# Performance work log

Hardware: AMD Instinct MI355X
Metric: run time of the kernel (lower is better)

Reference implementation:

```python
import jax, jax.numpy as jnp
import numpy as np

ALPHA, BETA, DELTA, TAU, GAMMA = 5.0, 0.6, 0.6, 0.5, 0.5
WINDOW, MOMENTUM = 5, 0.999


def setup_inputs() -> dict:
    key = jax.random.key(0)
    k1, k2 = jax.random.split(key)
    B, C, H, W = 32, 256, 64, 64
    F = jax.random.normal(k1, (B, C, H, W), dtype=jnp.float32)
    S = jnp.eye(C, dtype=jnp.float32)          # EMA similarity buffer (initialized as identity)
    U = jax.random.uniform(k2, (B, C), dtype=jnp.float32)  # replaces torch.bernoulli draw
    return {"F": F, "S": S, "U": U}


def _avg_pool(x, win):
    p = win // 2
    s = jax.lax.reduce_window(x, 0.0, jax.lax.add,
                              (1, 1, win, win), (1, 1, 1, 1),
                              [(0, 0), (0, 0), (p, p), (p, p)])
    return s / (win * win)


def _lrd_mask(F, U):
    # Local Response Density sampling -> boolean mask M [B, C]
    B, C, H, W = F.shape
    a = jax.nn.sigmoid(F.mean(axis=(2, 3)))                     # [B, C]
    max_vals = F.reshape(B, C, -1).max(axis=-1)[:, :, None, None]
    M_bin = (F >= DELTA * max_vals).astype(F.dtype)             # [B, C, H, W]
    density = _avg_pool(M_bin, WINDOW)
    d = (density >= TAU).astype(F.dtype).mean(axis=(2, 3))      # [B, C]
    s = a ** GAMMA * d ** (1.0 - GAMMA)
    s_max = s.max(axis=1, keepdims=True)
    prob = jax.nn.sigmoid(ALPHA * (s - BETA * s_max))
    return U < prob                                             # deterministic bernoulli


def _build_perm(m, S):
    # m: [C] bool selected mask, S: [C, C] similarity -> permutation [C] int32
    C = S.shape[0]
    idx = jnp.arange(C)
    unsel = ~m
    # for each channel, most-similar unselected channel (first max, like torch.argmax)
    masked = jnp.where(unsel[None, :], S, -jnp.inf)
    j = jnp.argmax(masked, axis=1)                              # [C]
    perm = jnp.where(m, j, idx)                                 # perm[selected] = j
    targets = jnp.where(m, j, C)                                # C is out-of-range -> dropped
    perm = perm.at[targets].set(idx, mode='drop')               # perm[j] = selected
    valid = m.any() & unsel.any()
    return jnp.where(valid, perm, idx)


def reference(F, S, U):
    B, C, H, W = F.shape
    # EMA update of channel similarity buffer (no_grad in original)
    F_flat = F.reshape(B, C, -1)
    F_norm = F_flat / (jnp.linalg.norm(F_flat, axis=2, keepdims=True) + 1e-6)
    S_batch = jnp.einsum('bcn,bdn->bcd', F_norm, F_norm).mean(axis=0)
    S_new = jax.lax.stop_gradient(MOMENTUM * S + (1.0 - MOMENTUM) * S_batch)
    # LRD sampling mask and per-sample channel-swap permutation
    M = _lrd_mask(jax.lax.stop_gradient(F), U)                  # [B, C] bool
    perm = jax.vmap(_build_perm, in_axes=(0, None))(M, S_new)   # [B, C]
    # structure-aware channel exchange (gather along channel dim)
    gidx = jnp.broadcast_to(perm[:, :, None, None], (B, C, H, W))
    return jnp.take_along_axis(F, gidx, axis=1)
```

## Files before the change

kernel.cpp:

```cpp
#include <hip/hip_runtime.h>
#include <math.h>

#define BB 32
#define CC 256
#define HH 64
#define WW 64
#define NN 4096

__inline__ __device__ float waveReduceSum(float v) {
    #pragma unroll
    for (int off = 32; off > 0; off >>= 1) v += __shfl_xor(v, off);
    return v;
}
__inline__ __device__ float waveReduceMax(float v) {
    #pragma unroll
    for (int off = 32; off > 0; off >>= 1) v = fmaxf(v, __shfl_xor(v, off));
    return v;
}

__global__ __launch_bounds__(256) void k_prep(const float* __restrict__ F,
                                              float* __restrict__ inv_norm,
                                              float* __restrict__ s_score) {
    const int plane = blockIdx.x;
    const int tid = threadIdx.x;
    __shared__ float bin[4096];
    __shared__ float rowsum[4096];
    __shared__ float swS[4], swQ[4], swM[4];

    const float4* src = (const float4*)(F + (size_t)plane * NN);
    float4 v[4];
    float sum = 0.f, ssq = 0.f, mx = -INFINITY;
    #pragma unroll
    for (int q = 0; q < 4; ++q) {
        v[q] = src[tid + q * 256];
        sum += v[q].x + v[q].y + v[q].z + v[q].w;
        ssq += v[q].x * v[q].x + v[q].y * v[q].y + v[q].z * v[q].z + v[q].w * v[q].w;
        mx = fmaxf(mx, fmaxf(fmaxf(v[q].x, v[q].y), fmaxf(v[q].z, v[q].w)));
    }
    sum = waveReduceSum(sum);
    ssq = waveReduceSum(ssq);
    mx  = waveReduceMax(mx);
    const int w = tid >> 6, ln = tid & 63;
    if (ln == 0) { swS[w] = sum; swQ[w] = ssq; swM[w] = mx; }
    __syncthreads();
    if (tid == 0) {
        swS[0] = swS[0] + swS[1] + swS[2] + swS[3];
        swQ[0] = swQ[0] + swQ[1] + swQ[2] + swQ[3];
        swM[0] = fmaxf(fmaxf(swM[0], swM[1]), fmaxf(swM[2], swM[3]));
    }
    __syncthreads();
    const float totsum = swS[0];
    const float totssq = swQ[0];
    const float thr = 0.6f * swM[0];

    #pragma unroll
    for (int q = 0; q < 4; ++q) {
        const int base = (tid + q * 256) * 4;
        bin[base + 0] = (v[q].x >= thr) ? 1.f : 0.f;
        bin[base + 1] = (v[q].y >= thr) ? 1.f : 0.f;
        bin[base + 2] = (v[q].z >= thr) ? 1.f : 0.f;
        bin[base + 3] = (v[q].w >= thr) ? 1.f : 0.f;
    }
    __syncthreads();

    #pragma unroll
    for (int q = 0; q < 16; ++q) {
        const int p = tid + q * 256;
        const int h = p >> 6, x = p & 63;
        float s5 = 0.f;
        #pragma unroll
        for (int dw = -2; dw <= 2; ++dw) {
            const int xx = x + dw;
            if (xx >= 0 && xx < 64) s5 += bin[h * 64 + xx];
        }
        rowsum[p] = s5;
    }
    __syncthreads();

    int cge = 0;
    #pragma unroll
    for (int q = 0; q < 16; ++q) {
        const int p = tid + q * 256;
        const int h = p >> 6, x = p & 63;
        float cnt = 0.f;
        #pragma unroll
        for (int dh = -2; dh <= 2; ++dh) {
            const int hh = h + dh;
            if (hh >= 0 && hh < 64) cnt += rowsum[hh * 64 + x];
        }
        if (cnt >= 12.5f) cge++;
    }
    float cf = waveReduceSum((float)cge);
    __syncthreads();
    if (ln == 0) swS[w] = cf;
    __syncthreads();
    if (tid == 0) {
        const float total = swS[0] + swS[1] + swS[2] + swS[3];
        const float d = total / 4096.f;
        const float a = 1.f / (1.f + expf(-(totsum / 4096.f)));
        s_score[plane] = sqrtf(a) * sqrtf(d);
        inv_norm[plane] = 1.f / (sqrtf(totssq) + 1e-6f);
    }
}

__global__ __launch_bounds__(256) void k_gram(const float* __restrict__ F,
                                              const float* __restrict__ inv_norm,
                                              float* __restrict__ S_part,
                                              int csh) {
    static const int TI[10] = {0,0,0,0,1,1,1,2,2,3};
    static const int TJ[10] = {0,1,2,3,1,2,3,2,3,3};
    const int t  = blockIdx.x;
    const int bc = blockIdx.y;
    const int b = bc >> csh, chunk = bc & ((1 << csh) - 1);
    const int ti = TI[t], tj = TJ[t];
    const int k0 = chunk << (12 - csh);
    const int iters = 128 >> csh;

    __shared__ float As[32][68];
    __shared__ float Bs[32][68];

    const int tid = threadIdx.x;
    const int lrow = tid >> 2;
    const int kgrp = tid & 3;
    const float* Fb = F + (size_t)b * CC * NN;
    const float scaleA = inv_norm[b * CC + ti * 64 + lrow];
    const float scaleB = inv_norm[b * CC + tj * 64 + lrow];
    const float* gA = Fb + (size_t)(ti * 64 + lrow) * NN + k0 + kgrp * 8;
    const float* gB = Fb + (size_t)(tj * 64 + lrow) * NN + k0 + kgrp * 8;

    const int r0 = (tid >> 4) << 2;
    const int c0 = (tid & 15) << 2;

    float accL2[16];
    #pragma unroll
    for (int e = 0; e < 16; ++e) accL2[e] = 0.f;

    for (int s = 0; s < iters; ++s) {
        const float4 a0 = *(const float4*)(gA);
        const float4 a1 = *(const float4*)(gA + 4);
        const float4 b0 = *(const float4*)(gB);
        const float4 b1 = *(const float4*)(gB + 4);
        __syncthreads();
        const int kb = kgrp * 8;
        As[kb + 0][lrow] = a0.x * scaleA; As[kb + 1][lrow] = a0.y * scaleA;
        As[kb + 2][lrow] = a0.z * scaleA; As[kb + 3][lrow] = a0.w * scaleA;
        As[kb + 4][lrow] = a1.x * scaleA; As[kb + 5][lrow] = a1.y * scaleA;
        As[kb + 6][lrow] = a1.z * scaleA; As[kb + 7][lrow] = a1.w * scaleA;
        Bs[kb + 0][lrow] = b0.x * scaleB; Bs[kb + 1][lrow] = b0.y * scaleB;
        Bs[kb + 2][lrow] = b0.z * scaleB; Bs[kb + 3][lrow] = b0.w * scaleB;
        Bs[kb + 4][lrow] = b1.x * scaleB; Bs[kb + 5][lrow] = b1.y * scaleB;
        Bs[kb + 6][lrow] = b1.z * scaleB; Bs[kb + 7][lrow] = b1.w * scaleB;
        __syncthreads();

        float accL1[16];
        #pragma unroll
        for (int e = 0; e < 16; ++e) accL1[e] = 0.f;
        #pragma unroll
        for (int kk = 0; kk < 32; ++kk) {
            const float4 av = *(const float4*)&As[kk][r0];
            const float4 bv = *(const float4*)&Bs[kk][c0];
            const float ar[4] = {av.x, av.y, av.z, av.w};
            const float br[4] = {bv.x, bv.y, bv.z, bv.w};
            #pragma unroll
            for (int rr = 0; rr < 4; ++rr)
                #pragma unroll
                for (int cc = 0; cc < 4; ++cc)
                    accL1[rr * 4 + cc] += ar[rr] * br[cc];
        }
        #pragma unroll
        for (int e = 0; e < 16; ++e) accL2[e] += accL1[e];
        gA += 32; gB += 32;
    }

    float* dst = S_part + (size_t)(bc * 10 + t) * 4096;
    #pragma unroll
    for (int rr = 0; rr < 4; ++rr)
        #pragma unroll
        for (int cc = 0; cc < 4; ++cc)
            dst[(r0 + rr) * 64 + (c0 + cc)] = accL2[rr * 4 + cc];
}

__global__ __launch_bounds__(256) void k_snew(const float* __restrict__ S_part,
                                              const float* __restrict__ S_old,
                                              float* __restrict__ S_new,
                                              int npart) {
    const int c = blockIdx.x;
    const int d = threadIdx.x;
    if (d < c) return;
    static const int tmap[16] = {0,1,2,3, -1,4,5,6, -1,-1,7,8, -1,-1,-1,9};
    const int t = tmap[((c >> 6) << 2) | (d >> 6)];
    const int r = c & 63, col = d & 63;
    const float* base = S_part + (size_t)t * 4096 + r * 64 + col;
    double sum = 0.0;
    for (int p = 0; p < npart; ++p) sum += (double)base[(size_t)p * 40960];
    const float sb = (float)(sum * (1.0 / 32.0));
    S_new[c * 256 + d] = 0.999f * S_old[c * 256 + d] + 0.001f * sb;
    if (d != c)
        S_new[d * 256 + c] = 0.999f * S_old[d * 256 + c] + 0.001f * sb;
}

__global__ __launch_bounds__(256) void k_perm(const float* __restrict__ s_score,
                                              const float* __restrict__ U,
                                              const float* __restrict__ S_new,
                                              int* __restrict__ perm_g) {
    const int b = blockIdx.x;
    const int c = threadIdx.x;
    __shared__ float red[256];
    __shared__ int m[256];
    __shared__ int jj[256];
    __shared__ int perm[256];

    const float s = s_score[b * 256 + c];
    red[c] = s; __syncthreads();
    for (int off = 128; off > 0; off >>= 1) {
        if (c < off) red[c] = fmaxf(red[c], red[c + off]);
        __syncthreads();
    }
    const float smax = red[0];
    __syncthreads();

    const float prob = 1.f / (1.f + expf(-5.f * (s - 0.6f * smax)));
    const int mi = (U[b * 256 + c] < prob) ? 1 : 0;
    m[c] = mi;
    red[c] = (float)mi;
    __syncthreads();
    for (int off = 128; off > 0; off >>= 1) {
        if (c < off) red[c] += red[c + off];
        __syncthreads();
    }
    const int cnt = (int)red[0];

    float best = -INFINITY; int bj = 0;
    const float* row = S_new + c * 256;
    for (int d2 = 0; d2 < 256; ++d2) {
        const float v = row[d2];
        if (!m[d2] && v > best) { best = v; bj = d2; }
    }
    jj[c] = bj;
    perm[c] = mi ? bj : c;
    __syncthreads();

    const int valid = (cnt > 0) && (cnt < 256);
    if (c == 0 && valid) {
        for (int q = 0; q < 256; ++q)
            if (m[q]) perm[jj[q]] = q;
    }
    __syncthreads();
    perm_g[b * 256 + c] = valid ? perm[c] : c;
}

__global__ __launch_bounds__(256) void k_gather(const float* __restrict__ F,
                                                const int* __restrict__ perm_g,
                                                float* __restrict__ out) {
    const int plane = blockIdx.x;
    const int b = plane >> 8;
    const int p = perm_g[plane];
    const float4* src = (const float4*)(F + ((size_t)b * 256 + p) * NN);
    float4* dst = (float4*)(out + (size_t)plane * NN);
    const int tid = threadIdx.x;
    #pragma unroll
    for (int q = 0; q < 4; ++q) dst[tid + q * 256] = src[tid + q * 256];
}

extern "C" void kernel_launch(void* const* d_in, const int* in_sizes, int n_in,
                              void* d_out, int out_size, void* d_ws, size_t ws_size,
                              hipStream_t stream) {
    const float* F = (const float*)d_in[0];
    const float* S = (const float*)d_in[1];
    const float* U = (const float*)d_in[2];
    float* out = (float*)d_out;

    const size_t need4 = (size_t)128 * 10 * 4096 * 4 + (3 * 8192 + 65536) * 4 + (1 << 16);
    const int csh = (ws_size >= need4) ? 2 : 1;
    const int nch = 1 << csh;
    const int npart = 32 * nch;

    char* ws = (char*)d_ws;
    size_t off = 0;
    float* S_part  = (float*)(ws + off); off += (size_t)npart * 10 * 4096 * 4;
    float* inv_nrm = (float*)(ws + off); off += 8192 * 4;
    float* s_score = (float*)(ws + off); off += 8192 * 4;
    float* S_new   = (float*)(ws + off); off += 65536 * 4;
    int*   perm    = (int*)  (ws + off); off += 8192 * 4;

    k_prep  <<<8192, 256, 0, stream>>>(F, inv_nrm, s_score);
    k_gram  <<<dim3(10, npart), 256, 0, stream>>>(F, inv_nrm, S_part, csh);
    k_snew  <<<256, 256, 0, stream>>>(S_part, S, S_new, npart);
    k_perm  <<<32, 256, 0, stream>>>(s_score, U, S_new, perm);
    k_gather<<<8192, 256, 0, stream>>>(F, perm, out);
}
```

Before: 489.2 us.

## Use 128x128 gram tiles with 8x8 register blocking and prefetched loads

The Gram kernel now computes three 128x128 upper-triangular tiles per batch chunk instead of ten 64x64 tiles. Each thread holds an 8x8 accumulator block, the next K-slice is loaded into registers while the current one is computed, and the inverse-norm scaling is applied once at the output instead of at every shared-memory store. Split-K can go up to 8 chunks when the workspace allows, and the reduction kernel is adapted with two accumulators. The goal is more arithmetic per shared-memory load and fewer redundant global reads, at the cost of higher register pressure (64 accumulators) and a larger partial-sum buffer.

Result: slower. 517.4 us (+5.8%).

```diff
diff --git a/kernel.cpp b/kernel.cpp
--- a/kernel.cpp
+++ b/kernel.cpp
@@ -6,6 +6,9 @@
 #define HH 64
 #define WW 64
 #define NN 4096
+
+#define KSTEP 32
+#define SROW  140
 
 __inline__ __device__ float waveReduceSum(float v) {
     #pragma unroll
@@ -107,77 +110,94 @@
                                               const float* __restrict__ inv_norm,
                                               float* __restrict__ S_part,
                                               int csh) {
-    static const int TI[10] = {0,0,0,0,1,1,1,2,2,3};
-    static const int TJ[10] = {0,1,2,3,1,2,3,2,3,3};
     const int t  = blockIdx.x;
     const int bc = blockIdx.y;
     const int b = bc >> csh, chunk = bc & ((1 << csh) - 1);
-    const int ti = TI[t], tj = TJ[t];
     const int k0 = chunk << (12 - csh);
-    const int iters = 128 >> csh;
-
-    __shared__ float As[32][68];
-    __shared__ float Bs[32][68];
+    const int iters = (4096 >> csh) / KSTEP;
+    const int IA = (t == 2) ? 1 : 0;
+    const int JB = (t == 0) ? 0 : 1;
+
+    __shared__ float As[KSTEP * SROW];
+    __shared__ float Bs[KSTEP * SROW];
 
     const int tid = threadIdx.x;
-    const int lrow = tid >> 2;
-    const int kgrp = tid & 3;
-    const float* Fb = F + (size_t)b * CC * NN;
-    const float scaleA = inv_norm[b * CC + ti * 64 + lrow];
-    const float scaleB = inv_norm[b * CC + tj * 64 + lrow];
-    const float* gA = Fb + (size_t)(ti * 64 + lrow) * NN + k0 + kgrp * 8;
-    const float* gB = Fb + (size_t)(tj * 64 + lrow) * NN + k0 + kgrp * 8;
-
-    const int r0 = (tid >> 4) << 2;
-    const int c0 = (tid & 15) << 2;
-
-    float accL2[16];
-    #pragma unroll
-    for (int e = 0; e < 16; ++e) accL2[e] = 0.f;
+    const int u = tid & 7;
+    const int rbase = tid >> 3;
+
+    const float* FA = F + (size_t)b * CC * NN + (size_t)(IA * 128) * NN;
+    const float* FB = F + (size_t)b * CC * NN + (size_t)(JB * 128) * NN;
+
+    const int r0 = (tid >> 4) << 3;
+    const int c0 = (tid & 15) << 3;
+    const int cA = r0 + ((r0 >> 5) << 2);
+    const int cB = c0 + ((c0 >> 5) << 2);
+
+    float acc[64];
+    #pragma unroll
+    for (int e = 0; e < 64; ++e) acc[e] = 0.f;
+
+    float4 stA[4], stB[4];
+    {
+        #pragma unroll
+        for (int p = 0; p < 4; ++p) {
+            const int row = p * 32 + rbase;
+            stA[p] = *(const float4*)(FA + (size_t)row * NN + k0 + u * 4);
+            stB[p] = *(const float4*)(FB + (size_t)row * NN + k0 + u * 4);
+        }
+    }
 
     for (int s = 0; s < iters; ++s) {
-        const float4 a0 = *(const float4*)(gA);
-        const float4 a1 = *(const float4*)(gA + 4);
-        const float4 b0 = *(const float4*)(gB);
-        const float4 b1 = *(const float4*)(gB + 4);
         __syncthreads();
-        const int kb = kgrp * 8;
-        As[kb + 0][lrow] = a0.x * scaleA; As[kb + 1][lrow] = a0.y * scaleA;
-        As[kb + 2][lrow] = a0.z * scaleA; As[kb + 3][lrow] = a0.w * scaleA;
-        As[kb + 4][lrow] = a1.x * scaleA; As[kb + 5][lrow] = a1.y * scaleA;
-        As[kb + 6][lrow] = a1.z * scaleA; As[kb + 7][lrow] = a1.w * scaleA;
-        Bs[kb + 0][lrow] = b0.x * scaleB; Bs[kb + 1][lrow] = b0.y * scaleB;
-        Bs[kb + 2][lrow] = b0.z * scaleB; Bs[kb + 3][lrow] = b0.w * scaleB;
-        Bs[kb + 4][lrow] = b1.x * scaleB; Bs[kb + 5][lrow] = b1.y * scaleB;
-        Bs[kb + 6][lrow] = b1.z * scaleB; Bs[kb + 7][lrow] = b1.w * scaleB;
+        #pragma unroll
+        for (int p = 0; p < 4; ++p) {
+            const int row = p * 32 + rbase;
+            const int col = row + ((row >> 5) << 2);
+            const float* va = (const float*)&stA[p];
+            const float* vb = (const float*)&stB[p];
+            #pragma unroll
+            for (int j = 0; j < 4; ++j) {
+                As[(u * 4 + j) * SROW + col] = va[j];
+                Bs[(u * 4 + j) * SROW + col] = vb[j];
+            }
+        }
         __syncthreads();
-
-        float accL1[16];
-        #pragma unroll
-        for (int e = 0; e < 16; ++e) accL1[e] = 0.f;
-        #pragma unroll
-        for (int kk = 0; kk < 32; ++kk) {
-            const float4 av = *(const float4*)&As[kk][r0];
-            const float4 bv = *(const float4*)&Bs[kk][c0];
-            const float ar[4] = {av.x, av.y, av.z, av.w};
-            const float br[4] = {bv.x, bv.y, bv.z, bv.w};
+        if (s + 1 < iters) {
+            const int kw = k0 + (s + 1) * KSTEP;
             #pragma unroll
-            for (int rr = 0; rr < 4; ++rr)
+            for (int p = 0; p < 4; ++p) {
+                const int row = p * 32 + rbase;
+                stA[p] = *(const float4*)(FA + (size_t)row * NN + kw + u * 4);
+                stB[p] = *(const float4*)(FB + (size_t)row * NN + kw + u * 4);
+            }
+        }
+        #pragma unroll
+        for (int kk = 0; kk < KSTEP; ++kk) {
+            const float4 a0 = *(const float4*)(As + kk * SROW + cA);
+            const float4 a1 = *(const float4*)(As + kk * SROW + cA + 4);
+            const float4 b0 = *(const float4*)(Bs + kk * SROW + cB);
+            const float4 b1 = *(const float4*)(Bs + kk * SROW + cB + 4);
+            const float ar[8] = {a0.x,a0.y,a0.z,a0.w,a1.x,a1.y,a1.z,a1.w};
+            const float br[8] = {b0.x,b0.y,b0.z,b0.w,b1.x,b1.y,b1.z,b1.w};
+            #pragma unroll
+            for (int rr = 0; rr < 8; ++rr)
                 #pragma unroll
-                for (int cc = 0; cc < 4; ++cc)
-                    accL1[rr * 4 + cc] += ar[rr] * br[cc];
-        }
-        #pragma unroll
-        for (int e = 0; e < 16; ++e) accL2[e] += accL1[e];
-        gA += 32; gB += 32;
-    }
-
-    float* dst = S_part + (size_t)(bc * 10 + t) * 4096;
-    #pragma unroll
-    for (int rr = 0; rr < 4; ++rr)
-        #pragma unroll
-        for (int cc = 0; cc < 4; ++cc)
-            dst[(r0 + rr) * 64 + (c0 + cc)] = accL2[rr * 4 + cc];
+                for (int cc = 0; cc < 8; ++cc)
+                    acc[rr * 8 + cc] = fmaf(ar[rr], br[cc], acc[rr * 8 + cc]);
+        }
+    }
+
+    const float* invA = inv_norm + b * CC + IA * 128;
+    const float* invB = inv_norm + b * CC + JB * 128;
+    float sA[8], sB[8];
+    #pragma unroll
+    for (int e = 0; e < 8; ++e) { sA[e] = invA[r0 + e]; sB[e] = invB[c0 + e]; }
+    float* dst = S_part + ((size_t)bc * 3 + t) * 16384;
+    #pragma unroll
+    for (int rr = 0; rr < 8; ++rr)
+        #pragma unroll
+        for (int cc = 0; cc < 8; ++cc)
+            dst[(r0 + rr) * 128 + (c0 + cc)] = acc[rr * 8 + cc] * sA[rr] * sB[cc];
 }
 
 __global__ __launch_bounds__(256) void k_snew(const float* __restrict__ S_part,
@@ -187,13 +207,17 @@
     const int c = blockIdx.x;
     const int d = threadIdx.x;
     if (d < c) return;
-    static const int tmap[16] = {0,1,2,3, -1,4,5,6, -1,-1,7,8, -1,-1,-1,9};
-    const int t = tmap[((c >> 6) << 2) | (d >> 6)];
-    const int r = c & 63, col = d & 63;
-    const float* base = S_part + (size_t)t * 4096 + r * 64 + col;
-    double sum = 0.0;
-    for (int p = 0; p < npart; ++p) sum += (double)base[(size_t)p * 40960];
-    const float sb = (float)(sum * (1.0 / 32.0));
+    const int t = (c >> 7) + (d >> 7);
+    const int r = c & 127, col = d & 127;
+    const float* base = S_part + (size_t)t * 16384 + (size_t)r * 128 + col;
+    double s0 = 0.0, s1 = 0.0;
+    int p = 0;
+    for (; p + 1 < npart; p += 2) {
+        s0 += (double)base[(size_t)p * 49152];
+        s1 += (double)base[(size_t)(p + 1) * 49152];
+    }
+    for (; p < npart; ++p) s0 += (double)base[(size_t)p * 49152];
+    const float sb = (float)((s0 + s1) * (1.0 / 32.0));
     S_new[c * 256 + d] = 0.999f * S_old[c * 256 + d] + 0.001f * sb;
     if (d != c)
         S_new[d * 256 + c] = 0.999f * S_old[d * 256 + c] + 0.001f * sb;
@@ -270,21 +294,22 @@
     const float* U = (const float*)d_in[2];
     float* out = (float*)d_out;
 
-    const size_t need4 = (size_t)128 * 10 * 4096 * 4 + (3 * 8192 + 65536) * 4 + (1 << 16);
-    const int csh = (ws_size >= need4) ? 2 : 1;
-    const int nch = 1 << csh;
-    const int npart = 32 * nch;
+    const size_t extras = (size_t)(3 * 8192 + 65536) * 4 + 65536;
+    int csh = 1;
+    if (ws_size >= (size_t)(32 << 3) * 3 * 16384 * 4 + extras) csh = 3;
+    else if (ws_size >= (size_t)(32 << 2) * 3 * 16384 * 4 + extras) csh = 2;
+    const int npart = 32 << csh;
 
     char* ws = (char*)d_ws;
     size_t off = 0;
-    float* S_part  = (float*)(ws + off); off += (size_t)npart * 10 * 4096 * 4;
+    float* S_part  = (float*)(ws + off); off += (size_t)npart * 3 * 16384 * 4;
     float* inv_nrm = (float*)(ws + off); off += 8192 * 4;
     float* s_score = (float*)(ws + off); off += 8192 * 4;
     float* S_new   = (float*)(ws + off); off += 65536 * 4;
     int*   perm    = (int*)  (ws + off); off += 8192 * 4;
 
     k_prep  <<<8192, 256, 0, stream>>>(F, inv_nrm, s_score);
-    k_gram  <<<dim3(10, npart), 256, 0, stream>>>(F, inv_nrm, S_part, csh);
+    k_gram  <<<dim3(3, npart), 256, 0, stream>>>(F, inv_nrm, S_part, csh);
     k_snew  <<<256, 256, 0, stream>>>(S_part, S, S_new, npart);
     k_perm  <<<32, 256, 0, stream>>>(s_score, U, S_new, perm);
     k_gather<<<8192, 256, 0, stream>>>(F, perm, out);
```
